# Kernel tuning notes

Hardware: AMD Instinct MI355X
Metric: run time of the kernel (lower is better)

## Reference

```python
import jax, jax.numpy as jnp
import numpy as np

T, B, E, H = 2048, 4, 1024, 16
HD = E // H
SCALING = 0.125  # 1/sqrt(64)
NEG_INF = -1e9


def setup_inputs() -> dict:
    key = jax.random.key(0)
    ks = jax.random.split(key, 6)
    query = jax.random.normal(ks[0], (T, B, E), dtype=jnp.float32)
    key_padding_mask = jnp.zeros((B, T), dtype=bool)  # no padded keys
    attn_mask = jax.random.normal(ks[1], (T, T), dtype=jnp.float32)
    W_in = jax.random.normal(ks[2], (3 * E, E), dtype=jnp.float32) * (1.0 / np.sqrt(E))
    b_in = jax.random.normal(ks[3], (3 * E,), dtype=jnp.float32) * 0.02
    W_out = jax.random.normal(ks[4], (E, E), dtype=jnp.float32) * (1.0 / np.sqrt(E))
    b_out = jax.random.normal(ks[5], (E,), dtype=jnp.float32) * 0.02
    return {"query": query, "key_padding_mask": key_padding_mask, "attn_mask": attn_mask,
            "W_in": W_in, "b_in": b_in, "W_out": W_out, "b_out": b_out}


def reference(query, key_padding_mask, attn_mask, W_in, b_in, W_out, b_out):
    t, b, e = query.shape
    # fused QKV projection: (T,B,3E)
    proj = jnp.einsum('tbe,fe->tbf', query, W_in) + b_in
    q, k, v = jnp.split(proj, 3, axis=-1)
    # (T,B,E) -> (T,B,H,Hd); torch's view(T, B*H, Hd) splits E as (H,Hd) per batch
    q = (q * SCALING).reshape(t, b, H, HD)
    k = k.reshape(t, b, H, HD)
    v = v.reshape(t, b, H, HD)
    # full score matrix, (B,H,T,S)
    scores = jnp.einsum('tbhd,sbhd->bhts', q, k)
    scores = scores + attn_mask[None, None, :, :]  # float attn_mask is added
    scores = jnp.where(key_padding_mask[:, None, None, :], NEG_INF, scores)
    w = jax.nn.softmax(scores.astype(jnp.float32), axis=-1).astype(query.dtype)
    attn = jnp.einsum('bhts,sbhd->tbhd', w, v).reshape(t, b, e)
    return jnp.einsum('tbe,fe->tbf', attn, W_out) + b_out
```

## Files before the change

### kernel.cpp

```cpp
#include <hip/hip_runtime.h>
#include <hip/hip_bf16.h>


typedef __attribute__((ext_vector_type(8))) short short8;
typedef __attribute__((ext_vector_type(4))) float f32x4;
typedef __attribute__((ext_vector_type(2))) float f32x2;
typedef __attribute__((ext_vector_type(16))) float f32x16;
typedef __attribute__((ext_vector_type(8))) unsigned short u16x8;
typedef __attribute__((ext_vector_type(4))) unsigned short u16x4;
typedef __attribute__((ext_vector_type(4))) unsigned int u32x4;
typedef __attribute__((ext_vector_type(4))) float fl4;

#define MFMA16(a,b,c) __builtin_amdgcn_mfma_f32_16x16x32_bf16((a),(b),(c),0,0,0)
#define MFMA32(a,b,c) __builtin_amdgcn_mfma_f32_32x32x16_bf16((a),(b),(c),0,0,0)

#define GLDS16(g,l) __builtin_amdgcn_global_load_lds( \
    (__attribute__((address_space(1))) const void*)(g), \
    (__attribute__((address_space(3))) void*)(l), 16, 0, 0)

#define VEXP2(x) __builtin_amdgcn_exp2f(x)

__device__ __forceinline__ unsigned short bf16us(float x) {
  __hip_bfloat16 h = __float2bfloat16(x);
  return __builtin_bit_cast(unsigned short, h);
}
__device__ __forceinline__ unsigned cvtpk(float lo, float hi) {
  unsigned r;
  asm("v_cvt_pk_bf16_f32 %0, %1, %2" : "=v"(r) : "v"(lo), "v"(hi));
  return r;
}
__device__ __forceinline__ void plswap(unsigned& a, unsigned& b) {
  asm volatile("v_permlane32_swap_b32 %0, %1" : "+v"(a), "+v"(b));
}

__global__ __launch_bounds__(256) void f2bf3_kernel(
    const float* __restrict__ qin, const float* __restrict__ wi,
    const float* __restrict__ wo, unsigned short* __restrict__ oq,
    unsigned short* __restrict__ owi, unsigned short* __restrict__ owo) {
  int bid = blockIdx.x;
  const float* in;
  unsigned short* out;
  int base;
  if (bid < 8192)       { in = qin; out = oq;  base = bid; }
  else if (bid < 11264) { in = wi;  out = owi; base = bid - 8192; }
  else                  { in = wo;  out = owo; base = bid - 11264; }
  int i = (base * 256 + threadIdx.x) * 4;
  fl4 v = *(const fl4*)&in[i];
  u16x4 o;
#pragma unroll
  for (int j = 0; j < 4; ++j) o[j] = bf16us(v[j]);
  *(u16x4*)&out[i] = o;
}

__global__ __launch_bounds__(256) void maskpack_kernel(const float* __restrict__ in,
                                                       float* __restrict__ out) {
  int id = blockIdx.x * 256 + threadIdx.x;
  int lane = id & 63;
  int r4   = (id >> 6) & 7;
  int qt   = (id >> 9) & 63;
  int it   = id >> 15;
  int l31 = lane & 31, hv = lane >> 5;
  int q = qt * 32 + l31;
  int s = it * 64 + (r4 & 3) * 8 + 4 * hv + 32 * (r4 >> 2);
  fl4 v = *(const fl4*)&in[(size_t)q * 2048 + s];
  *(fl4*)&out[(size_t)id * 4] = v * 1.4426950408889634f;
}

template <int MODE>
__global__ __launch_bounds__(256) void gemm_bt(
    const unsigned short* __restrict__ A,
    const unsigned short* __restrict__ Bt,
    const float* __restrict__ bias,
    float* __restrict__ outF,
    unsigned short* __restrict__ qp, unsigned short* __restrict__ kp,
    unsigned short* __restrict__ vp,
    int M, int N, int K) {
  __shared__ unsigned short lA[3][128 * 32];
  __shared__ unsigned short lB[3][128 * 32];
  const int tid = threadIdx.x;
  const int wave = tid >> 6, lane = tid & 63;
  const int lrow = lane & 15, lk = lane >> 4;
  const int wr = wave >> 1, wc = wave & 1;
  const int m0 = blockIdx.y * 128, n0 = blockIdx.x * 128;
  const int rA = lane >> 2;
  const int gsw = ((lane & 3) ^ ((rA >> 1) & 3)) * 8;
  const int gkey = (lrow >> 1) & 3;

#define GSTAGE(KT, BUF)                                                        \
  do {                                                                         \
    _Pragma("unroll")                                                          \
    for (int j_ = 0; j_ < 2; ++j_) {                                           \
      int li_ = wave * 2 + j_;                                                 \
      GLDS16(A + (size_t)(m0 + li_ * 16 + rA) * K + (KT) + gsw,                \
             &lA[BUF][li_ * 512]);                                             \
      GLDS16(Bt + (size_t)(n0 + li_ * 16 + rA) * K + (KT) + gsw,               \
             &lB[BUF][li_ * 512]);                                             \
    }                                                                          \
  } while (0)

  f32x4 acc[4][4] = {};
  const int nsteps = K >> 5;

  GSTAGE(0, 0);
  asm volatile("" ::: "memory");
  GSTAGE(32, 1);

  const int roffA = (wr * 64 + lrow) * 32 + (lk ^ gkey) * 8;
  const int roffB = (wc * 64 + lrow) * 32 + (lk ^ gkey) * 8;

  for (int t = 0; t < nsteps; ++t) {
    const int cur = t % 3;
    if (t < nsteps - 1) asm volatile("s_waitcnt vmcnt(4)" ::: "memory");
    else                asm volatile("s_waitcnt vmcnt(0)" ::: "memory");
    __builtin_amdgcn_s_barrier();
    if (t + 2 < nsteps) GSTAGE((t + 2) * 32, (t + 2) % 3);
    asm volatile("" ::: "memory");

    short8 af[4], bf[4];
#pragma unroll
    for (int mt = 0; mt < 4; ++mt)
      af[mt] = *(const short8*)&lA[cur][roffA + mt * 512];
#pragma unroll
    for (int nt = 0; nt < 4; ++nt)
      bf[nt] = *(const short8*)&lB[cur][roffB + nt * 512];
    __builtin_amdgcn_s_setprio(1);
#pragma unroll
    for (int mt = 0; mt < 4; ++mt)
#pragma unroll
      for (int nt = 0; nt < 4; ++nt)
        acc[mt][nt] = MFMA16(af[mt], bf[nt], acc[mt][nt]);
    __builtin_amdgcn_s_setprio(0);

    asm volatile("s_waitcnt lgkmcnt(0)" ::: "memory");
  }
#undef GSTAGE

#pragma unroll
  for (int mt = 0; mt < 4; ++mt) {
#pragma unroll
    for (int nt = 0; nt < 4; ++nt) {
      int c = n0 + wc * 64 + nt * 16 + lrow;
      float bb = bias[c];
      int rbase = m0 + wr * 64 + mt * 16 + lk * 4;
#pragma unroll
      for (int j = 0; j < 4; ++j) {
        float val = acc[mt][nt][j] + bb;
        int row = rbase + j;
        if (MODE == 0) {
          int t = row >> 2, b = row & 3;
          int f = c;
          unsigned short* dst;
          float sc = 1.0f;
          if (f < 1024) { dst = qp; sc = 0.18033688011112042f; }
          else if (f < 2048) { dst = kp; f -= 1024; }
          else { dst = vp; f -= 2048; }
          int h = f >> 6, d = f & 63;
          dst[(((size_t)(b * 16 + h)) * 2048 + t) * 64 + d] = bf16us(val * sc);
        } else {
          outF[(size_t)row * N + c] = val;
        }
      }
    }
  }
}

__global__ __launch_bounds__(256) void transpose_v(const unsigned short* __restrict__ v,
                                                   unsigned short* __restrict__ vt) {
  __shared__ unsigned short tile[64][72];
  int bh = blockIdx.y, t0 = blockIdx.x * 64;
  int tid = threadIdx.x;
#pragma unroll
  for (int i = 0; i < 2; ++i) {
    int idx = tid + i * 256;
    int r = idx >> 3, c = (idx & 7) * 8;
    *(u16x8*)&tile[r][c] = *(const u16x8*)&v[((size_t)bh * 2048 + t0 + r) * 64 + c];
  }
  __syncthreads();
#pragma unroll
  for (int i = 0; i < 2; ++i) {
    int idx = tid + i * 256;
    int d = idx >> 3, tc = (idx & 7) * 8;
    u16x8 o;
#pragma unroll
    for (int j = 0; j < 8; ++j) o[j] = tile[tc + j][d];
    *(u16x8*)&vt[((size_t)bh * 64 + d) * 2048 + t0 + tc] = o;
  }
}

__global__ __launch_bounds__(512) void attn_fwd(
    const unsigned short* __restrict__ q,
    const unsigned short* __restrict__ kk,
    const unsigned short* __restrict__ vt,
    const float* __restrict__ maskP,
    unsigned short* __restrict__ attn_out) {
  __shared__ unsigned short Kb[2][64 * 64];
  __shared__ unsigned short Vb[2][64 * 64];
  const int tid = threadIdx.x, w = tid >> 6, lane = tid & 63;
  const int l31 = lane & 31, hv = lane >> 5;
  const int rx7 = l31 & 7;
  const int bh = blockIdx.y, b = bh >> 4, hed = bh & 15;
  const int qt0 = blockIdx.x * 256;

  const unsigned short* qbase = q + ((size_t)bh * 2048 + qt0) * 64;
  const unsigned short* kbase = kk + (size_t)bh * 2048 * 64;
  const unsigned short* vbase = vt + (size_t)bh * 64 * 2048;
  const float* mP = maskP + (size_t)(blockIdx.x * 8 + w) * 2048 + lane * 4;

  short8 qf[4];
#pragma unroll
  for (int kc = 0; kc < 4; ++kc)
    qf[kc] = *(const short8*)(qbase + (size_t)(w * 32 + l31) * 64 + kc * 16 + hv * 8);
  asm volatile("" ::: "memory");

  const int sr = w * 8 + (lane >> 3);
  const int sc = ((lane & 7) ^ ((lane >> 3) & 7)) * 8;
  const int ldsoff = w * 512;

  GLDS16(kbase + (size_t)sr * 64 + sc, &Kb[0][ldsoff]);
  GLDS16(vbase + (size_t)sr * 2048 + sc, &Vb[0][ldsoff]);
  asm volatile("" ::: "memory");

  f32x16 S0, S1;
#pragma unroll
  for (int r4 = 0; r4 < 4; ++r4) {
    fl4 a = *(const fl4*)(mP + r4 * 256);
    fl4 bq = *(const fl4*)(mP + 1024 + r4 * 256);
#pragma unroll
    for (int j = 0; j < 4; ++j) { S0[r4 * 4 + j] = a[j]; S1[r4 * 4 + j] = bq[j]; }
  }

  f32x16 o0 = {}, o1 = {};
  f32x2 lsum2 = {0.f, 0.f};

  for (int it = 0; it < 32; ++it) {
    const int st = it * 64;
    const int cur = it & 1;
    asm volatile("s_waitcnt vmcnt(8)" ::: "memory");
    __builtin_amdgcn_s_barrier();

    if (it < 31) {
      const int s1 = st + 64;
      GLDS16(kbase + (size_t)(s1 + sr) * 64 + sc, &Kb[cur ^ 1][ldsoff]);
      GLDS16(vbase + (size_t)sr * 2048 + s1 + sc, &Vb[cur ^ 1][ldsoff]);
    }
    asm volatile("" ::: "memory");

    __builtin_amdgcn_s_setprio(1);
#pragma unroll
    for (int kc = 0; kc < 4; ++kc) {
      const int g0 = ((kc * 2 + hv) ^ rx7) * 8;
      short8 kf0 = *(const short8*)&Kb[cur][l31 * 64 + g0];
      short8 kf1 = *(const short8*)&Kb[cur][(32 + l31) * 64 + g0];
      S0 = MFMA32(kf0, qf[kc], S0);
      S1 = MFMA32(kf1, qf[kc], S1);
    }
    __builtin_amdgcn_s_setprio(0);

    unsigned pk[8];
    short8 pa[4];
#pragma unroll
    for (int i = 0; i < 8; ++i) {
      float e0 = VEXP2(S0[2 * i]), e1 = VEXP2(S0[2 * i + 1]);
      lsum2 += (f32x2){e0, e1};
      pk[i] = cvtpk(e0, e1);
    }
    plswap(pk[0], pk[2]); plswap(pk[1], pk[3]);
    plswap(pk[4], pk[6]); plswap(pk[5], pk[7]);
    pa[0] = __builtin_bit_cast(short8, (u32x4){pk[0], pk[1], pk[2], pk[3]});
    pa[1] = __builtin_bit_cast(short8, (u32x4){pk[4], pk[5], pk[6], pk[7]});
#pragma unroll
    for (int i = 0; i < 8; ++i) {
      float e0 = VEXP2(S1[2 * i]), e1 = VEXP2(S1[2 * i + 1]);
      lsum2 += (f32x2){e0, e1};
      pk[i] = cvtpk(e0, e1);
    }
    plswap(pk[0], pk[2]); plswap(pk[1], pk[3]);
    plswap(pk[4], pk[6]); plswap(pk[5], pk[7]);
    pa[2] = __builtin_bit_cast(short8, (u32x4){pk[0], pk[1], pk[2], pk[3]});
    pa[3] = __builtin_bit_cast(short8, (u32x4){pk[4], pk[5], pk[6], pk[7]});

    __builtin_amdgcn_s_setprio(1);
#pragma unroll
    for (int scc = 0; scc < 4; ++scc) {
      const int g = ((scc * 2 + hv) ^ rx7) * 8;
      short8 vf0 = *(const short8*)&Vb[cur][l31 * 64 + g];
      short8 vf1 = *(const short8*)&Vb[cur][(32 + l31) * 64 + g];
      o0 = MFMA32(pa[scc], vf0, o0);
      o1 = MFMA32(pa[scc], vf1, o1);
    }
    __builtin_amdgcn_s_setprio(0);

    if (it < 31) {
      const float* mb = mP + (size_t)(it + 1) * 131072;
#pragma unroll
      for (int r4 = 0; r4 < 4; ++r4) {
        fl4 a = *(const fl4*)(mb + r4 * 256);
        fl4 bq = *(const fl4*)(mb + 1024 + r4 * 256);
#pragma unroll
        for (int j = 0; j < 4; ++j) { S0[r4 * 4 + j] = a[j]; S1[r4 * 4 + j] = bq[j]; }
      }
    }

    asm volatile("s_waitcnt lgkmcnt(0)" ::: "memory");
  }

  float lsum = lsum2[0] + lsum2[1];
  lsum += __shfl_xor(lsum, 32);
  f32x16 rl;
#pragma unroll
  for (int r = 0; r < 16; ++r) {
    const int qq = (r & 3) + 8 * (r >> 2) + 4 * hv;
    rl[r] = 1.0f / __shfl(lsum, qq);
  }
#pragma unroll
  for (int r = 0; r < 16; ++r) {
    int t = qt0 + w * 32 + (r & 3) + 8 * (r >> 2) + 4 * hv;
    unsigned short* orow = attn_out + ((size_t)t * 4 + b) * 1024 + hed * 64 + l31;
    orow[0]  = bf16us(o0[r] * rl[r]);
    orow[32] = bf16us(o1[r] * rl[r]);
  }
}

extern "C" void kernel_launch(void* const* d_in, const int* in_sizes, int n_in,
                              void* d_out, int out_size, void* d_ws, size_t ws_size,
                              hipStream_t stream) {
  if (n_in < 7) return;
  const float* query = (const float*)d_in[0];
  const float* mask  = (const float*)d_in[2];
  const float* W_in  = (const float*)d_in[3];
  const float* b_in  = (const float*)d_in[4];
  const float* W_out = (const float*)d_in[5];
  const float* b_out = (const float*)d_in[6];
  float* out = (float*)d_out;

  char* ws = (char*)d_ws;
  unsigned short* Xbf    = (unsigned short*)(ws);
  unsigned short* Winbf  = (unsigned short*)(ws + 16777216);
  unsigned short* Woutbf = (unsigned short*)(ws + 23068672);
  unsigned short* qbf    = (unsigned short*)(ws + 25165824);
  unsigned short* kbf    = (unsigned short*)(ws + 41943040);
  unsigned short* vbf    = (unsigned short*)(ws + 58720256);
  unsigned short* vtbf   = (unsigned short*)(ws + 75497472);
  unsigned short* abf    = (unsigned short*)(ws + 92274688);
  float* maskPf          = (float*)(ws);
  if (ws_size < 109051904) return;

  f2bf3_kernel<<<12288, 256, 0, stream>>>(query, W_in, W_out, Xbf, Winbf, Woutbf);

  gemm_bt<0><<<dim3(24, 64), 256, 0, stream>>>(Xbf, Winbf, b_in, nullptr,
                                               qbf, kbf, vbf, 8192, 3072, 1024);
  transpose_v<<<dim3(32, 64), 256, 0, stream>>>(vbf, vtbf);
  maskpack_kernel<<<4096, 256, 0, stream>>>(mask, maskPf);
  attn_fwd<<<dim3(8, 64), 512, 0, stream>>>(qbf, kbf, vtbf, maskPf, abf);
  gemm_bt<1><<<dim3(8, 64), 256, 0, stream>>>(abf, Woutbf, b_out, out,
                                              nullptr, nullptr, nullptr, 8192, 1024, 1024);
}
```

Baseline: 230.1 us.

## Fuse V transpose into QKV GEMM epilogue and merge mask packing into prep kernel

The QKV projection GEMM now writes V straight into the transposed (bh, d, t) layout by staging the bias-added tile in shared memory and doing coalesced 16-byte stores. This removes the separate transpose_v kernel and its 16 MB round trip through global memory. Mask packing is folded into the bf16 conversion kernel, so two launches become one. The V blocks pay for this with an extra LDS pass and two barriers in the epilogue, and the workspace layout is rearranged so the mask buffer no longer overlaps the bf16 inputs.

```diff
diff --git a/kernel.cpp b/kernel.cpp
--- a/kernel.cpp
+++ b/kernel.cpp
@@ -33,37 +33,37 @@
   asm volatile("v_permlane32_swap_b32 %0, %1" : "+v"(a), "+v"(b));
 }
 
-__global__ __launch_bounds__(256) void f2bf3_kernel(
+__global__ __launch_bounds__(256) void prep_kernel(
     const float* __restrict__ qin, const float* __restrict__ wi,
-    const float* __restrict__ wo, unsigned short* __restrict__ oq,
-    unsigned short* __restrict__ owi, unsigned short* __restrict__ owo) {
+    const float* __restrict__ wo, const float* __restrict__ mask,
+    unsigned short* __restrict__ oq, unsigned short* __restrict__ owi,
+    unsigned short* __restrict__ owo, float* __restrict__ omask) {
   int bid = blockIdx.x;
-  const float* in;
-  unsigned short* out;
-  int base;
-  if (bid < 8192)       { in = qin; out = oq;  base = bid; }
-  else if (bid < 11264) { in = wi;  out = owi; base = bid - 8192; }
-  else                  { in = wo;  out = owo; base = bid - 11264; }
-  int i = (base * 256 + threadIdx.x) * 4;
-  fl4 v = *(const fl4*)&in[i];
-  u16x4 o;
-#pragma unroll
-  for (int j = 0; j < 4; ++j) o[j] = bf16us(v[j]);
-  *(u16x4*)&out[i] = o;
-}
-
-__global__ __launch_bounds__(256) void maskpack_kernel(const float* __restrict__ in,
-                                                       float* __restrict__ out) {
-  int id = blockIdx.x * 256 + threadIdx.x;
-  int lane = id & 63;
-  int r4   = (id >> 6) & 7;
-  int qt   = (id >> 9) & 63;
-  int it   = id >> 15;
-  int l31 = lane & 31, hv = lane >> 5;
-  int q = qt * 32 + l31;
-  int s = it * 64 + (r4 & 3) * 8 + 4 * hv + 32 * (r4 >> 2);
-  fl4 v = *(const fl4*)&in[(size_t)q * 2048 + s];
-  *(fl4*)&out[(size_t)id * 4] = v * 1.4426950408889634f;
+  if (bid < 12288) {
+    const float* in;
+    unsigned short* out;
+    int base;
+    if (bid < 8192)       { in = qin; out = oq;  base = bid; }
+    else if (bid < 11264) { in = wi;  out = owi; base = bid - 8192; }
+    else                  { in = wo;  out = owo; base = bid - 11264; }
+    int i = (base * 256 + threadIdx.x) * 4;
+    fl4 v = *(const fl4*)&in[i];
+    u16x4 o;
+#pragma unroll
+    for (int j = 0; j < 4; ++j) o[j] = bf16us(v[j]);
+    *(u16x4*)&out[i] = o;
+  } else {
+    int id = (bid - 12288) * 256 + threadIdx.x;
+    int lane = id & 63;
+    int r4   = (id >> 6) & 7;
+    int qt   = (id >> 9) & 63;
+    int it   = id >> 15;
+    int l31 = lane & 31, hv = lane >> 5;
+    int q = qt * 32 + l31;
+    int s = it * 64 + (r4 & 3) * 8 + 4 * hv + 32 * (r4 >> 2);
+    fl4 v = *(const fl4*)&mask[(size_t)q * 2048 + s];
+    *(fl4*)&omask[(size_t)id * 4] = v * 1.4426950408889634f;
+  }
 }
 
 template <int MODE>
@@ -75,8 +75,9 @@
     unsigned short* __restrict__ qp, unsigned short* __restrict__ kp,
     unsigned short* __restrict__ vp,
     int M, int N, int K) {
-  __shared__ unsigned short lA[3][128 * 32];
-  __shared__ unsigned short lB[3][128 * 32];
+  __shared__ unsigned short smem[24576];
+#define LA(BUF) (&smem[(BUF) * 4096])
+#define LB(BUF) (&smem[12288 + (BUF) * 4096])
   const int tid = threadIdx.x;
   const int wave = tid >> 6, lane = tid & 63;
   const int lrow = lane & 15, lk = lane >> 4;
@@ -92,9 +93,9 @@
     for (int j_ = 0; j_ < 2; ++j_) {                                           \
       int li_ = wave * 2 + j_;                                                 \
       GLDS16(A + (size_t)(m0 + li_ * 16 + rA) * K + (KT) + gsw,                \
-             &lA[BUF][li_ * 512]);                                             \
+             &LA(BUF)[li_ * 512]);                                             \
       GLDS16(Bt + (size_t)(n0 + li_ * 16 + rA) * K + (KT) + gsw,               \
-             &lB[BUF][li_ * 512]);                                             \
+             &LB(BUF)[li_ * 512]);                                             \
     }                                                                          \
   } while (0)
 
@@ -119,10 +120,10 @@
     short8 af[4], bf[4];
 #pragma unroll
     for (int mt = 0; mt < 4; ++mt)
-      af[mt] = *(const short8*)&lA[cur][roffA + mt * 512];
+      af[mt] = *(const short8*)&LA(cur)[roffA + mt * 512];
 #pragma unroll
     for (int nt = 0; nt < 4; ++nt)
-      bf[nt] = *(const short8*)&lB[cur][roffB + nt * 512];
+      bf[nt] = *(const short8*)&LB(cur)[roffB + nt * 512];
     __builtin_amdgcn_s_setprio(1);
 #pragma unroll
     for (int mt = 0; mt < 4; ++mt)
@@ -134,6 +135,37 @@
     asm volatile("s_waitcnt lgkmcnt(0)" ::: "memory");
   }
 #undef GSTAGE
+
+  if (MODE == 0 && n0 >= 2048) {
+    unsigned short (*tile)[130] = (unsigned short(*)[130])smem;
+    __builtin_amdgcn_s_barrier();
+#pragma unroll
+    for (int mt = 0; mt < 4; ++mt)
+#pragma unroll
+      for (int nt = 0; nt < 4; ++nt) {
+        int cl = wc * 64 + nt * 16 + lrow;
+        float bb = bias[n0 + cl];
+        int rb = wr * 64 + mt * 16 + lk * 4;
+        u16x4 pkv;
+#pragma unroll
+        for (int j = 0; j < 4; ++j) pkv[j] = bf16us(acc[mt][nt][j] + bb);
+        *(u16x4*)&tile[cl][rb] = pkv;
+      }
+    __builtin_amdgcn_s_barrier();
+    const int h0 = (n0 - 2048) >> 6;
+    const int t0 = m0 >> 2;
+#pragma unroll
+    for (int i = 0; i < 8; ++i) {
+      int wid = tid * 8 + i;
+      int cl = wid >> 4, b = (wid >> 2) & 3, tc = wid & 3;
+      int h = h0 + (cl >> 6), d = cl & 63;
+      u16x8 o;
+#pragma unroll
+      for (int j = 0; j < 8; ++j) o[j] = tile[cl][(tc * 8 + j) * 4 + b];
+      *(u16x8*)&vp[(((size_t)(b * 16 + h)) * 64 + d) * 2048 + t0 + tc * 8] = o;
+    }
+    return;
+  }
 
 #pragma unroll
   for (int mt = 0; mt < 4; ++mt) {
@@ -152,8 +184,7 @@
           unsigned short* dst;
           float sc = 1.0f;
           if (f < 1024) { dst = qp; sc = 0.18033688011112042f; }
-          else if (f < 2048) { dst = kp; f -= 1024; }
-          else { dst = vp; f -= 2048; }
+          else { dst = kp; f -= 1024; }
           int h = f >> 6, d = f & 63;
           dst[(((size_t)(b * 16 + h)) * 2048 + t) * 64 + d] = bf16us(val * sc);
         } else {
@@ -161,29 +192,6 @@
         }
       }
     }
-  }
-}
-
-__global__ __launch_bounds__(256) void transpose_v(const unsigned short* __restrict__ v,
-                                                   unsigned short* __restrict__ vt) {
-  __shared__ unsigned short tile[64][72];
-  int bh = blockIdx.y, t0 = blockIdx.x * 64;
-  int tid = threadIdx.x;
-#pragma unroll
-  for (int i = 0; i < 2; ++i) {
-    int idx = tid + i * 256;
-    int r = idx >> 3, c = (idx & 7) * 8;
-    *(u16x8*)&tile[r][c] = *(const u16x8*)&v[((size_t)bh * 2048 + t0 + r) * 64 + c];
-  }
-  __syncthreads();
-#pragma unroll
-  for (int i = 0; i < 2; ++i) {
-    int idx = tid + i * 256;
-    int d = idx >> 3, tc = (idx & 7) * 8;
-    u16x8 o;
-#pragma unroll
-    for (int j = 0; j < 8; ++j) o[j] = tile[tc + j][d];
-    *(u16x8*)&vt[((size_t)bh * 64 + d) * 2048 + t0 + tc] = o;
   }
 }
 
@@ -339,18 +347,15 @@
   unsigned short* Woutbf = (unsigned short*)(ws + 23068672);
   unsigned short* qbf    = (unsigned short*)(ws + 25165824);
   unsigned short* kbf    = (unsigned short*)(ws + 41943040);
-  unsigned short* vbf    = (unsigned short*)(ws + 58720256);
-  unsigned short* vtbf   = (unsigned short*)(ws + 75497472);
-  unsigned short* abf    = (unsigned short*)(ws + 92274688);
-  float* maskPf          = (float*)(ws);
+  unsigned short* vtbf   = (unsigned short*)(ws + 58720256);
+  unsigned short* abf    = (unsigned short*)(ws + 75497472);
+  float* maskPf          = (float*)(ws + 92274688);
   if (ws_size < 109051904) return;
 
-  f2bf3_kernel<<<12288, 256, 0, stream>>>(query, W_in, W_out, Xbf, Winbf, Woutbf);
-
+  prep_kernel<<<16384, 256, 0, stream>>>(query, W_in, W_out, mask,
+                                         Xbf, Winbf, Woutbf, maskPf);
   gemm_bt<0><<<dim3(24, 64), 256, 0, stream>>>(Xbf, Winbf, b_in, nullptr,
-                                               qbf, kbf, vbf, 8192, 3072, 1024);
-  transpose_v<<<dim3(32, 64), 256, 0, stream>>>(vbf, vtbf);
-  maskpack_kernel<<<4096, 256, 0, stream>>>(mask, maskPf);
+                                               qbf, kbf, vtbf, 8192, 3072, 1024);
   attn_fwd<<<dim3(8, 64), 512, 0, stream>>>(qbf, kbf, vtbf, maskPf, abf);
   gemm_bt<1><<<dim3(8, 64), 256, 0, stream>>>(abf, Woutbf, b_out, out,
                                               nullptr, nullptr, nullptr, 8192, 1024, 1024);
```

After: 215.5 us. -6.3%, faster.
